# Optimization experiments

Measured on AMD Instinct MI355X. Metric: run time of the kernel, lower is better.

The kernel has to match this reference:

```python
import jax, jax.numpy as jnp
import numpy as np

D = 512       # model_dim
H = 8         # num_heads
DH = D // H   # dim_per_head
LN_EPS = 1e-5


def setup_inputs() -> dict:
    key = jax.random.key(0)
    ks = jax.random.split(key, 10)
    B, S = 2, 2048
    s = D ** -0.5
    return {
        "query": jax.random.normal(ks[0], (B, S, D), jnp.float32),
        "key":   jax.random.normal(ks[1], (B, S, D), jnp.float32),
        "value": jax.random.normal(ks[2], (B, S, D), jnp.float32),
        # torch Linear weights: [out, in], y = x @ W.T
        "Wq": jax.random.normal(ks[3], (D, D), jnp.float32) * s,
        "Wk": jax.random.normal(ks[4], (D, D), jnp.float32) * s,
        "Wv": jax.random.normal(ks[5], (D, D), jnp.float32) * s,
        "Wo": jax.random.normal(ks[6], (D, D), jnp.float32) * s,
        "bo": jnp.zeros((D,), jnp.float32),
        "gamma": jnp.ones((D,), jnp.float32),
        "beta":  jnp.zeros((D,), jnp.float32),
    }


def _layer_norm(x, gamma, beta):
    mu = jnp.mean(x, axis=-1, keepdims=True)
    var = jnp.var(x, axis=-1, keepdims=True)
    return (x - mu) * jax.lax.rsqrt(var + LN_EPS) * gamma + beta


def reference(query, key, value, Wq, Wk, Wv, Wo, bo, gamma, beta):
    B, S, _ = query.shape
    residual = query
    # projections (torch Linear: x @ W.T), split heads -> [B, H, S, DH]
    q = (query @ Wq.T).reshape(B, S, H, DH).transpose(0, 2, 1, 3)
    k = (key   @ Wk.T).reshape(B, S, H, DH).transpose(0, 2, 1, 3)
    v = (value @ Wv.T).reshape(B, S, H, DH).transpose(0, 2, 1, 3)
    scale = DH ** -0.5
    scores = jnp.einsum('bhqd,bhkd->bhqk', q, k) * scale
    attention = jax.nn.softmax(scores, axis=-1)
    context = jnp.einsum('bhqk,bhkd->bhqd', attention, v)
    context = context.transpose(0, 2, 1, 3).reshape(B, S, D)
    output = context @ Wo.T + bo
    output = _layer_norm(residual + output, gamma, beta)
    # original returns attention as [B*H, S, S]
    return output, attention.reshape(B * H, S, S)
```

## Files before the change

kernel.cpp:

```cpp
#include <hip/hip_runtime.h>

#define B_ 2
#define S_ 2048
#define D_ 512
#define H_ 8
#define DH_ 64

typedef __bf16 bf16_8 __attribute__((ext_vector_type(8)));
typedef float f32x4 __attribute__((ext_vector_type(4)));

union BfPack4 { ushort4 u; __bf16 h[4]; };

__global__ __launch_bounds__(256) void proj_qkv(
    const float* __restrict__ Xq, const float* __restrict__ Xk, const float* __restrict__ Xv,
    const float* __restrict__ Wq, const float* __restrict__ Wk, const float* __restrict__ Wv,
    __bf16* __restrict__ Qb, __bf16* __restrict__ Kb, __bf16* __restrict__ Vt)
{
    const int z = blockIdx.z;
    const float* X = (z == 0) ? Xq : (z == 1) ? Xk : Xv;
    const float* W = (z == 0) ? Wq : (z == 1) ? Wk : Wv;
    const int m0 = blockIdx.x * 64;
    const int n0 = blockIdx.y * 64;

    __shared__ __bf16 Xs[64][72];
    __shared__ __bf16 Ws[64][72];

    const int tid = threadIdx.x;
    const int w = tid >> 6, lane = tid & 63;
    const int quad = lane >> 4, mc = lane & 15;

    int rr[4], cc[4];
    for (int i = 0; i < 4; ++i) { int e = tid + i * 256; rr[i] = e >> 4; cc[i] = (e & 15) * 4; }

    f32x4 acc[4] = {};
    float4 xr[4], wv[4];
    for (int i = 0; i < 4; ++i) {
        xr[i] = *reinterpret_cast<const float4*>(&X[(size_t)(m0 + rr[i]) * 512 + cc[i]]);
        wv[i] = *reinterpret_cast<const float4*>(&W[(size_t)(n0 + rr[i]) * 512 + cc[i]]);
    }

    for (int kc = 0; kc < 512; kc += 64) {
        if (kc) __syncthreads();
        for (int i = 0; i < 4; ++i) {
            BfPack4 px, pw;
            px.h[0] = (__bf16)xr[i].x; px.h[1] = (__bf16)xr[i].y;
            px.h[2] = (__bf16)xr[i].z; px.h[3] = (__bf16)xr[i].w;
            *reinterpret_cast<ushort4*>(&Xs[rr[i]][cc[i]]) = px.u;
            pw.h[0] = (__bf16)wv[i].x; pw.h[1] = (__bf16)wv[i].y;
            pw.h[2] = (__bf16)wv[i].z; pw.h[3] = (__bf16)wv[i].w;
            *reinterpret_cast<ushort4*>(&Ws[rr[i]][cc[i]]) = pw.u;
        }
        __syncthreads();
        if (kc < 448) {
            for (int i = 0; i < 4; ++i) {
                xr[i] = *reinterpret_cast<const float4*>(&X[(size_t)(m0 + rr[i]) * 512 + kc + 64 + cc[i]]);
                wv[i] = *reinterpret_cast<const float4*>(&W[(size_t)(n0 + rr[i]) * 512 + kc + 64 + cc[i]]);
            }
        }
        for (int ks = 0; ks < 64; ks += 32) {
            bf16_8 a = *reinterpret_cast<const bf16_8*>(&Xs[w * 16 + mc][ks + quad * 8]);
            for (int tt = 0; tt < 4; ++tt) {
                bf16_8 bb = *reinterpret_cast<const bf16_8*>(&Ws[tt * 16 + mc][ks + quad * 8]);
                acc[tt] = __builtin_amdgcn_mfma_f32_16x16x32_bf16(a, bb, acc[tt], 0, 0, 0);
            }
        }
    }
    __syncthreads();
    const float scale = (z == 0) ? 0.125f : 1.0f;
    if (z < 2) {
        for (int tt = 0; tt < 4; ++tt)
            for (int r = 0; r < 4; ++r)
                Xs[w * 16 + quad * 4 + r][tt * 16 + mc] = (__bf16)(acc[tt][r] * scale);
    } else {
        for (int tt = 0; tt < 4; ++tt)
            for (int r = 0; r < 4; ++r)
                Xs[tt * 16 + mc][w * 16 + quad * 4 + r] = (__bf16)acc[tt][r];
    }
    __syncthreads();
    if (z < 2) {
        __bf16* out = (z == 0) ? Qb : Kb;
        for (int i = 0; i < 2; ++i) {
            int e = tid + i * 256;
            int r = e >> 3, c8 = (e & 7) * 8;
            *reinterpret_cast<uint4*>(&out[(size_t)(m0 + r) * 512 + n0 + c8]) =
                *reinterpret_cast<const uint4*>(&Xs[r][c8]);
        }
    } else {
        int b = m0 >> 11, s0 = m0 & 2047, h = n0 >> 6;
        for (int i = 0; i < 2; ++i) {
            int e = tid + i * 256;
            int r = e >> 3, c8 = (e & 7) * 8;
            *reinterpret_cast<uint4*>(&Vt[(((size_t)(b * H_ + h)) * DH_ + r) * S_ + s0 + c8]) =
                *reinterpret_cast<const uint4*>(&Xs[r][c8]);
        }
    }
}

__global__ __launch_bounds__(256) void attn_kernel(
    const __bf16* __restrict__ Qb, const __bf16* __restrict__ Kb, const __bf16* __restrict__ Vt,
    __bf16* __restrict__ Ctx, float* __restrict__ attn_out)
{
    const int qt = blockIdx.x;
    const int bh = blockIdx.y;
    const int b = bh >> 3, h = bh & 7;
    const int q0 = qt * 64;

    __shared__ __bf16 Qs[64][72];
    __shared__ __bf16 Ks[128][72];
    __shared__ __bf16 Ps[64][136];
    __shared__ __bf16 Vs[64][136];

    const int tid = threadIdx.x;
    const int w = tid >> 6, lane = tid & 63;
    const int quad = lane >> 4, mc = lane & 15;

    for (int i = 0; i < 2; ++i) {
        int e = tid + i * 256;
        int r = e >> 3, c8 = (e & 7) * 8;
        *reinterpret_cast<uint4*>(&Qs[r][c8]) =
            *reinterpret_cast<const uint4*>(&Qb[((size_t)b * S_ + q0 + r) * D_ + h * DH_ + c8]);
    }
    __syncthreads();
    const bf16_8 aq0 = *reinterpret_cast<const bf16_8*>(&Qs[w * 16 + mc][quad * 8]);
    const bf16_8 aq1 = *reinterpret_cast<const bf16_8*>(&Qs[w * 16 + mc][32 + quad * 8]);

    int kr[4], kcc[4], vr[4], vc[4];
    for (int i = 0; i < 4; ++i) {
        int e = tid + i * 256;
        kr[i] = e >> 3; kcc[i] = (e & 7) * 8;
        vr[i] = e >> 4; vc[i]  = (e & 15) * 8;
    }
    const __bf16* kp = Kb + (size_t)b * S_ * D_ + h * DH_;
    const __bf16* vp = Vt + (size_t)bh * DH_ * S_;

    float l[4] = {0.f, 0.f, 0.f, 0.f};

    uint4 kreg[4];
    for (int i = 0; i < 4; ++i)
        kreg[i] = *reinterpret_cast<const uint4*>(&kp[(size_t)kr[i] * D_ + kcc[i]]);

    for (int tc = 0; tc < 16; ++tc) {
        if (tc) __syncthreads();
        for (int i = 0; i < 4; ++i)
            *reinterpret_cast<uint4*>(&Ks[kr[i]][kcc[i]]) = kreg[i];
        __syncthreads();
        if (tc < 15) {
            for (int i = 0; i < 4; ++i)
                kreg[i] = *reinterpret_cast<const uint4*>(
                    &kp[(size_t)((tc + 1) * 128 + kr[i]) * D_ + kcc[i]]);
        }
        f32x4 s[8] = {};
        for (int ct = 0; ct < 8; ++ct) {
            bf16_8 b0 = *reinterpret_cast<const bf16_8*>(&Ks[ct * 16 + mc][quad * 8]);
            s[ct] = __builtin_amdgcn_mfma_f32_16x16x32_bf16(aq0, b0, s[ct], 0, 0, 0);
        }
        for (int ct = 0; ct < 8; ++ct) {
            bf16_8 b1 = *reinterpret_cast<const bf16_8*>(&Ks[ct * 16 + mc][32 + quad * 8]);
            s[ct] = __builtin_amdgcn_mfma_f32_16x16x32_bf16(aq1, b1, s[ct], 0, 0, 0);
        }
        for (int r = 0; r < 4; ++r) {
            float sum = __expf(s[0][r]) + __expf(s[1][r]) + __expf(s[2][r]) + __expf(s[3][r]) +
                        __expf(s[4][r]) + __expf(s[5][r]) + __expf(s[6][r]) + __expf(s[7][r]);
            for (int off = 1; off < 16; off <<= 1) sum += __shfl_xor(sum, off);
            l[r] += sum;
        }
    }
    float linv[4];
    for (int r = 0; r < 4; ++r) linv[r] = 1.f / l[r];

    uint4 vreg[4];
    for (int i = 0; i < 4; ++i) {
        kreg[i] = *reinterpret_cast<const uint4*>(&kp[(size_t)kr[i] * D_ + kcc[i]]);
        vreg[i] = *reinterpret_cast<const uint4*>(&vp[(size_t)vr[i] * S_ + vc[i]]);
    }
    f32x4 o[4] = {};
    for (int tc = 0; tc < 16; ++tc) {
        __syncthreads();
        for (int i = 0; i < 4; ++i) {
            *reinterpret_cast<uint4*>(&Ks[kr[i]][kcc[i]]) = kreg[i];
            *reinterpret_cast<uint4*>(&Vs[vr[i]][vc[i]]) = vreg[i];
        }
        __syncthreads();
        if (tc < 15) {
            for (int i = 0; i < 4; ++i) {
                kreg[i] = *reinterpret_cast<const uint4*>(
                    &kp[(size_t)((tc + 1) * 128 + kr[i]) * D_ + kcc[i]]);
                vreg[i] = *reinterpret_cast<const uint4*>(
                    &vp[(size_t)vr[i] * S_ + (tc + 1) * 128 + vc[i]]);
            }
        }
        f32x4 s[8] = {};
        for (int ct = 0; ct < 8; ++ct) {
            bf16_8 b0 = *reinterpret_cast<const bf16_8*>(&Ks[ct * 16 + mc][quad * 8]);
            s[ct] = __builtin_amdgcn_mfma_f32_16x16x32_bf16(aq0, b0, s[ct], 0, 0, 0);
        }
        for (int ct = 0; ct < 8; ++ct) {
            bf16_8 b1 = *reinterpret_cast<const bf16_8*>(&Ks[ct * 16 + mc][32 + quad * 8]);
            s[ct] = __builtin_amdgcn_mfma_f32_16x16x32_bf16(aq1, b1, s[ct], 0, 0, 0);
        }
        for (int ct = 0; ct < 8; ++ct)
            for (int r = 0; r < 4; ++r)
                Ps[w * 16 + quad * 4 + r][ct * 16 + mc] = (__bf16)(__expf(s[ct][r]) * linv[r]);
        const int kc = tc * 128;
        for (int i = 0; i < 4; ++i) {
            int r = w * 16 + i * 4 + quad;
            bf16_8 pv8 = *reinterpret_cast<const bf16_8*>(&Ps[r][mc * 8]);
            f32x4 lo, hi;
            lo[0] = (float)pv8[0]; lo[1] = (float)pv8[1]; lo[2] = (float)pv8[2]; lo[3] = (float)pv8[3];
            hi[0] = (float)pv8[4]; hi[1] = (float)pv8[5]; hi[2] = (float)pv8[6]; hi[3] = (float)pv8[7];
            float* dst = &attn_out[((size_t)bh * S_ + q0 + r) * S_ + kc + mc * 8];
            __builtin_nontemporal_store(lo, reinterpret_cast<f32x4*>(dst));
            __builtin_nontemporal_store(hi, reinterpret_cast<f32x4*>(dst + 4));
        }
        for (int ks = 0; ks < 128; ks += 32) {
            bf16_8 ap = *reinterpret_cast<const bf16_8*>(&Ps[w * 16 + mc][ks + quad * 8]);
            for (int tt = 0; tt < 4; ++tt) {
                bf16_8 bv = *reinterpret_cast<const bf16_8*>(&Vs[tt * 16 + mc][ks + quad * 8]);
                o[tt] = __builtin_amdgcn_mfma_f32_16x16x32_bf16(ap, bv, o[tt], 0, 0, 0);
            }
        }
    }
    __syncthreads();
    for (int tt = 0; tt < 4; ++tt)
        for (int r = 0; r < 4; ++r)
            Qs[w * 16 + quad * 4 + r][tt * 16 + mc] = (__bf16)o[tt][r];
    __syncthreads();
    for (int i = 0; i < 2; ++i) {
        int e = tid + i * 256;
        int r = e >> 3, c8 = (e & 7) * 8;
        *reinterpret_cast<uint4*>(&Ctx[((size_t)b * S_ + q0 + r) * D_ + h * DH_ + c8]) =
            *reinterpret_cast<const uint4*>(&Qs[r][c8]);
    }
}

__global__ __launch_bounds__(256) void oproj(
    const __bf16* __restrict__ Ctx, const float* __restrict__ Wo,
    const float* __restrict__ bo, const float* __restrict__ resid,
    float* __restrict__ Y)
{
    const int m0 = blockIdx.x * 64;
    const int n0 = blockIdx.y * 64;

    __shared__ __bf16 As[64][72];
    __shared__ __bf16 Bs[64][72];

    const int tid = threadIdx.x;
    const int w = tid >> 6, lane = tid & 63;
    const int quad = lane >> 4, mc = lane & 15;

    int ar[2], ac[2], wr2[4], wc2[4];
    for (int i = 0; i < 2; ++i) { int e = tid + i * 256; ar[i] = e >> 3; ac[i] = (e & 7) * 8; }
    for (int i = 0; i < 4; ++i) { int e = tid + i * 256; wr2[i] = e >> 4; wc2[i] = (e & 15) * 4; }

    uint4 areg[2];
    float4 wreg[4];
    for (int i = 0; i < 2; ++i)
        areg[i] = *reinterpret_cast<const uint4*>(&Ctx[(size_t)(m0 + ar[i]) * 512 + ac[i]]);
    for (int i = 0; i < 4; ++i)
        wreg[i] = *reinterpret_cast<const float4*>(&Wo[(size_t)(n0 + wr2[i]) * 512 + wc2[i]]);

    f32x4 acc[4] = {};
    for (int kc = 0; kc < 512; kc += 64) {
        if (kc) __syncthreads();
        for (int i = 0; i < 2; ++i)
            *reinterpret_cast<uint4*>(&As[ar[i]][ac[i]]) = areg[i];
        for (int i = 0; i < 4; ++i) {
            BfPack4 pw;
            pw.h[0] = (__bf16)wreg[i].x; pw.h[1] = (__bf16)wreg[i].y;
            pw.h[2] = (__bf16)wreg[i].z; pw.h[3] = (__bf16)wreg[i].w;
            *reinterpret_cast<ushort4*>(&Bs[wr2[i]][wc2[i]]) = pw.u;
        }
        __syncthreads();
        if (kc < 448) {
            for (int i = 0; i < 2; ++i)
                areg[i] = *reinterpret_cast<const uint4*>(&Ctx[(size_t)(m0 + ar[i]) * 512 + kc + 64 + ac[i]]);
            for (int i = 0; i < 4; ++i)
                wreg[i] = *reinterpret_cast<const float4*>(&Wo[(size_t)(n0 + wr2[i]) * 512 + kc + 64 + wc2[i]]);
        }
        for (int ks = 0; ks < 64; ks += 32) {
            bf16_8 a = *reinterpret_cast<const bf16_8*>(&As[w * 16 + mc][ks + quad * 8]);
            for (int tt = 0; tt < 4; ++tt) {
                bf16_8 bb = *reinterpret_cast<const bf16_8*>(&Bs[tt * 16 + mc][ks + quad * 8]);
                acc[tt] = __builtin_amdgcn_mfma_f32_16x16x32_bf16(a, bb, acc[tt], 0, 0, 0);
            }
        }
    }
    for (int tt = 0; tt < 4; ++tt) {
        int col = n0 + tt * 16 + mc;
        float bias = bo[col];
        for (int r = 0; r < 4; ++r) {
            int row = m0 + w * 16 + quad * 4 + r;
            Y[(size_t)row * 512 + col] = acc[tt][r] + bias + resid[(size_t)row * 512 + col];
        }
    }
}

__global__ __launch_bounds__(256) void ln_kernel(
    const float* __restrict__ Y, const float* __restrict__ gamma,
    const float* __restrict__ beta, float* __restrict__ out)
{
    const int row = blockIdx.x * 4 + (threadIdx.x >> 6);
    const int lane = threadIdx.x & 63;
    const float* y = &Y[(size_t)row * 512];
    float4 v0 = *reinterpret_cast<const float4*>(&y[lane * 8]);
    float4 v1 = *reinterpret_cast<const float4*>(&y[lane * 8 + 4]);
    float sum = v0.x + v0.y + v0.z + v0.w + v1.x + v1.y + v1.z + v1.w;
    float sq = v0.x * v0.x + v0.y * v0.y + v0.z * v0.z + v0.w * v0.w +
               v1.x * v1.x + v1.y * v1.y + v1.z * v1.z + v1.w * v1.w;
    for (int off = 1; off < 64; off <<= 1) {
        sum += __shfl_xor(sum, off);
        sq  += __shfl_xor(sq, off);
    }
    const float mean = sum * (1.f / 512.f);
    const float var = sq * (1.f / 512.f) - mean * mean;
    const float rstd = rsqrtf(var + 1e-5f);
    float4 g0 = *reinterpret_cast<const float4*>(&gamma[lane * 8]);
    float4 g1 = *reinterpret_cast<const float4*>(&gamma[lane * 8 + 4]);
    float4 b0 = *reinterpret_cast<const float4*>(&beta[lane * 8]);
    float4 b1 = *reinterpret_cast<const float4*>(&beta[lane * 8 + 4]);
    float4 o0, o1;
    o0.x = (v0.x - mean) * rstd * g0.x + b0.x;
    o0.y = (v0.y - mean) * rstd * g0.y + b0.y;
    o0.z = (v0.z - mean) * rstd * g0.z + b0.z;
    o0.w = (v0.w - mean) * rstd * g0.w + b0.w;
    o1.x = (v1.x - mean) * rstd * g1.x + b1.x;
    o1.y = (v1.y - mean) * rstd * g1.y + b1.y;
    o1.z = (v1.z - mean) * rstd * g1.z + b1.z;
    o1.w = (v1.w - mean) * rstd * g1.w + b1.w;
    *reinterpret_cast<float4*>(&out[(size_t)row * 512 + lane * 8]) = o0;
    *reinterpret_cast<float4*>(&out[(size_t)row * 512 + lane * 8 + 4]) = o1;
}

extern "C" void kernel_launch(void* const* d_in, const int* in_sizes, int n_in,
                              void* d_out, int out_size, void* d_ws, size_t ws_size,
                              hipStream_t stream)
{
    const float* query = (const float*)d_in[0];
    const float* key   = (const float*)d_in[1];
    const float* value = (const float*)d_in[2];
    const float* Wq    = (const float*)d_in[3];
    const float* Wk    = (const float*)d_in[4];
    const float* Wv    = (const float*)d_in[5];
    const float* Wo    = (const float*)d_in[6];
    const float* bo    = (const float*)d_in[7];
    const float* gamma = (const float*)d_in[8];
    const float* beta  = (const float*)d_in[9];

    float* out = (float*)d_out;
    float* attn_out = out + (size_t)B_ * S_ * D_;

    char* ws = (char*)d_ws;
    __bf16* Qb  = (__bf16*)(ws);
    __bf16* Kb  = (__bf16*)(ws + (4u << 20));
    __bf16* Vt  = (__bf16*)(ws + (8u << 20));
    __bf16* Ctx = (__bf16*)(ws + (12u << 20));
    float*  Y   = (float*)(ws + (16u << 20));

    proj_qkv<<<dim3(64, 8, 3), 256, 0, stream>>>(query, key, value, Wq, Wk, Wv, Qb, Kb, Vt);
    attn_kernel<<<dim3(32, 16), 256, 0, stream>>>(Qb, Kb, Vt, Ctx, attn_out);
    oproj<<<dim3(64, 8), 256, 0, stream>>>(Ctx, Wo, bo, query, Y);
    ln_kernel<<<1024, 256, 0, stream>>>(Y, gamma, beta, out);
}
```

Before: 456.7 us.

## Fuse softmax row-sum into single attention pass and defer normalization to rescale kernel

Removes the first QK^T pass that only computed softmax denominators. The attention kernel now accumulates row sums while computing exp(scores), uses the unnormalized probabilities for the PV matmul, and normalizes the context at the end. Unnormalized bf16 probabilities go to a workspace buffer, and a new rescale kernel multiplies them by 1/l and writes the fp32 attention output. This trades one full QK^T recompute for extra global traffic (a bf16 write plus a read of a B*H*S*S buffer) and an extra kernel launch. It also assumes the workspace is large enough for the added buffers.

```diff
diff --git a/kernel.cpp b/kernel.cpp
--- a/kernel.cpp
+++ b/kernel.cpp
@@ -8,6 +8,7 @@
 
 typedef __bf16 bf16_8 __attribute__((ext_vector_type(8)));
 typedef float f32x4 __attribute__((ext_vector_type(4)));
+typedef unsigned int u32x4 __attribute__((ext_vector_type(4)));
 
 union BfPack4 { ushort4 u; __bf16 h[4]; };
 
@@ -98,7 +99,7 @@
 
 __global__ __launch_bounds__(256) void attn_kernel(
     const __bf16* __restrict__ Qb, const __bf16* __restrict__ Kb, const __bf16* __restrict__ Vt,
-    __bf16* __restrict__ Ctx, float* __restrict__ attn_out)
+    __bf16* __restrict__ Ctx, __bf16* __restrict__ Pws, float* __restrict__ Linv)
 {
     const int qt = blockIdx.x;
     const int bh = blockIdx.y;
@@ -133,49 +134,17 @@
     const __bf16* kp = Kb + (size_t)b * S_ * D_ + h * DH_;
     const __bf16* vp = Vt + (size_t)bh * DH_ * S_;
 
-    float l[4] = {0.f, 0.f, 0.f, 0.f};
-
-    uint4 kreg[4];
-    for (int i = 0; i < 4; ++i)
-        kreg[i] = *reinterpret_cast<const uint4*>(&kp[(size_t)kr[i] * D_ + kcc[i]]);
-
-    for (int tc = 0; tc < 16; ++tc) {
-        if (tc) __syncthreads();
-        for (int i = 0; i < 4; ++i)
-            *reinterpret_cast<uint4*>(&Ks[kr[i]][kcc[i]]) = kreg[i];
-        __syncthreads();
-        if (tc < 15) {
-            for (int i = 0; i < 4; ++i)
-                kreg[i] = *reinterpret_cast<const uint4*>(
-                    &kp[(size_t)((tc + 1) * 128 + kr[i]) * D_ + kcc[i]]);
-        }
-        f32x4 s[8] = {};
-        for (int ct = 0; ct < 8; ++ct) {
-            bf16_8 b0 = *reinterpret_cast<const bf16_8*>(&Ks[ct * 16 + mc][quad * 8]);
-            s[ct] = __builtin_amdgcn_mfma_f32_16x16x32_bf16(aq0, b0, s[ct], 0, 0, 0);
-        }
-        for (int ct = 0; ct < 8; ++ct) {
-            bf16_8 b1 = *reinterpret_cast<const bf16_8*>(&Ks[ct * 16 + mc][32 + quad * 8]);
-            s[ct] = __builtin_amdgcn_mfma_f32_16x16x32_bf16(aq1, b1, s[ct], 0, 0, 0);
-        }
-        for (int r = 0; r < 4; ++r) {
-            float sum = __expf(s[0][r]) + __expf(s[1][r]) + __expf(s[2][r]) + __expf(s[3][r]) +
-                        __expf(s[4][r]) + __expf(s[5][r]) + __expf(s[6][r]) + __expf(s[7][r]);
-            for (int off = 1; off < 16; off <<= 1) sum += __shfl_xor(sum, off);
-            l[r] += sum;
-        }
-    }
-    float linv[4];
-    for (int r = 0; r < 4; ++r) linv[r] = 1.f / l[r];
-
-    uint4 vreg[4];
+    uint4 kreg[4], vreg[4];
     for (int i = 0; i < 4; ++i) {
         kreg[i] = *reinterpret_cast<const uint4*>(&kp[(size_t)kr[i] * D_ + kcc[i]]);
         vreg[i] = *reinterpret_cast<const uint4*>(&vp[(size_t)vr[i] * S_ + vc[i]]);
     }
+
+    float l[4] = {0.f, 0.f, 0.f, 0.f};
     f32x4 o[4] = {};
+
     for (int tc = 0; tc < 16; ++tc) {
-        __syncthreads();
+        if (tc) __syncthreads();
         for (int i = 0; i < 4; ++i) {
             *reinterpret_cast<uint4*>(&Ks[kr[i]][kcc[i]]) = kreg[i];
             *reinterpret_cast<uint4*>(&Vs[vr[i]][vc[i]]) = vreg[i];
@@ -199,18 +168,17 @@
             s[ct] = __builtin_amdgcn_mfma_f32_16x16x32_bf16(aq1, b1, s[ct], 0, 0, 0);
         }
         for (int ct = 0; ct < 8; ++ct)
-            for (int r = 0; r < 4; ++r)
-                Ps[w * 16 + quad * 4 + r][ct * 16 + mc] = (__bf16)(__expf(s[ct][r]) * linv[r]);
+            for (int r = 0; r < 4; ++r) {
+                float p = __expf(s[ct][r]);
+                l[r] += p;
+                Ps[w * 16 + quad * 4 + r][ct * 16 + mc] = (__bf16)p;
+            }
         const int kc = tc * 128;
         for (int i = 0; i < 4; ++i) {
             int r = w * 16 + i * 4 + quad;
-            bf16_8 pv8 = *reinterpret_cast<const bf16_8*>(&Ps[r][mc * 8]);
-            f32x4 lo, hi;
-            lo[0] = (float)pv8[0]; lo[1] = (float)pv8[1]; lo[2] = (float)pv8[2]; lo[3] = (float)pv8[3];
-            hi[0] = (float)pv8[4]; hi[1] = (float)pv8[5]; hi[2] = (float)pv8[6]; hi[3] = (float)pv8[7];
-            float* dst = &attn_out[((size_t)bh * S_ + q0 + r) * S_ + kc + mc * 8];
-            __builtin_nontemporal_store(lo, reinterpret_cast<f32x4*>(dst));
-            __builtin_nontemporal_store(hi, reinterpret_cast<f32x4*>(dst + 4));
+            u32x4 pu = *reinterpret_cast<const u32x4*>(&Ps[r][mc * 8]);
+            __builtin_nontemporal_store(pu, reinterpret_cast<u32x4*>(
+                &Pws[((size_t)bh * S_ + q0 + r) * S_ + kc + mc * 8]));
         }
         for (int ks = 0; ks < 128; ks += 32) {
             bf16_8 ap = *reinterpret_cast<const bf16_8*>(&Ps[w * 16 + mc][ks + quad * 8]);
@@ -220,10 +188,18 @@
             }
         }
     }
+    for (int r = 0; r < 4; ++r)
+        for (int off = 1; off < 16; off <<= 1) l[r] += __shfl_xor(l[r], off);
+    float linv[4];
+    for (int r = 0; r < 4; ++r) linv[r] = 1.f / l[r];
+    if (mc == 0)
+        for (int r = 0; r < 4; ++r)
+            Linv[(size_t)bh * S_ + q0 + w * 16 + quad * 4 + r] = linv[r];
+
     __syncthreads();
     for (int tt = 0; tt < 4; ++tt)
         for (int r = 0; r < 4; ++r)
-            Qs[w * 16 + quad * 4 + r][tt * 16 + mc] = (__bf16)o[tt][r];
+            Qs[w * 16 + quad * 4 + r][tt * 16 + mc] = (__bf16)(o[tt][r] * linv[r]);
     __syncthreads();
     for (int i = 0; i < 2; ++i) {
         int e = tid + i * 256;
@@ -231,6 +207,26 @@
         *reinterpret_cast<uint4*>(&Ctx[((size_t)b * S_ + q0 + r) * D_ + h * DH_ + c8]) =
             *reinterpret_cast<const uint4*>(&Qs[r][c8]);
     }
+}
+
+__global__ __launch_bounds__(256) void rescale_kernel(
+    const __bf16* __restrict__ Pws, const float* __restrict__ Linv,
+    float* __restrict__ attn_out)
+{
+    const int row = blockIdx.x;
+    const float s = Linv[row];
+    const int c = threadIdx.x * 8;
+    const size_t base = (size_t)row * S_ + c;
+    u32x4 pu = __builtin_nontemporal_load(reinterpret_cast<const u32x4*>(&Pws[base]));
+    const __bf16* p = reinterpret_cast<const __bf16*>(&pu);
+    f32x4 lo, hi;
+    for (int j = 0; j < 4; ++j) {
+        lo[j] = (float)p[j] * s;
+        hi[j] = (float)p[j + 4] * s;
+    }
+    float* dst = &attn_out[base];
+    __builtin_nontemporal_store(lo, reinterpret_cast<f32x4*>(dst));
+    __builtin_nontemporal_store(hi, reinterpret_cast<f32x4*>(dst + 4));
 }
 
 __global__ __launch_bounds__(256) void oproj(
@@ -355,9 +351,12 @@
     __bf16* Vt  = (__bf16*)(ws + (8u << 20));
     __bf16* Ctx = (__bf16*)(ws + (12u << 20));
     float*  Y   = (float*)(ws + (16u << 20));
+    float*  Linv= (float*)(ws + (24u << 20));
+    __bf16* Pws = (__bf16*)(ws + (32u << 20));
 
     proj_qkv<<<dim3(64, 8, 3), 256, 0, stream>>>(query, key, value, Wq, Wk, Wv, Qb, Kb, Vt);
-    attn_kernel<<<dim3(32, 16), 256, 0, stream>>>(Qb, Kb, Vt, Ctx, attn_out);
+    attn_kernel<<<dim3(32, 16), 256, 0, stream>>>(Qb, Kb, Vt, Ctx, Pws, Linv);
+    rescale_kernel<<<B_ * H_ * S_, 256, 0, stream>>>(Pws, Linv, attn_out);
     oproj<<<dim3(64, 8), 256, 0, stream>>>(Ctx, Wo, bo, query, Y);
     ln_kernel<<<1024, 256, 0, stream>>>(Y, gamma, beta, out);
 }
```

New measurement: 487.8 us. 6.8% more time.
